# Optimization experiments

Hardware: AMD Instinct MI355X
Metric: run time of the kernel (lower is better)

Reference implementation:

```python
import jax, jax.numpy as jnp
import numpy as np

THRESHOLD = 0.5
NEG_POS_RATIO = 3
ALPHA = 1.0
B, P, C, O = 128, 8732, 21, 32


def xy_to_cxcy(xy):
    return jnp.concatenate([(xy[..., 2:] + xy[..., :2]) / 2, xy[..., 2:] - xy[..., :2]], axis=-1)


def cxcy_to_xy(cxcy):
    return jnp.concatenate([cxcy[..., :2] - cxcy[..., 2:] / 2, cxcy[..., :2] + cxcy[..., 2:] / 2], axis=-1)


def cxcy_to_gcxgcy(cxcy, priors_cxcy):
    g_cxcy = (cxcy[..., :2] - priors_cxcy[..., :2]) / (priors_cxcy[..., 2:] / 10.0)
    g_wh = jnp.log(cxcy[..., 2:] / priors_cxcy[..., 2:]) * 5.0
    return jnp.concatenate([g_cxcy, g_wh], axis=-1)


def find_jaccard_overlap(set1, set2):
    # set1: [O,4] xy, set2: [P,4] xy -> [O,P]
    lo = jnp.maximum(set1[:, None, :2], set2[None, :, :2])
    hi = jnp.minimum(set1[:, None, 2:], set2[None, :, 2:])
    inter = jnp.prod(jnp.clip(hi - lo, 0.0), axis=-1)
    a1 = jnp.prod(set1[:, 2:] - set1[:, :2], axis=-1)
    a2 = jnp.prod(set2[:, 2:] - set2[:, :2], axis=-1)
    union = a1[:, None] + a2[None, :] - inter
    return inter / union


def setup_inputs() -> dict:
    key = jax.random.key(0)
    k0, k1, k2, k3, k4, k5, k6 = jax.random.split(key, 7)
    predicted_locs = jax.random.normal(k0, (B, P, 4), jnp.float32)
    predicted_scores = jax.random.normal(k1, (B, P, C), jnp.float32)
    centers = jax.random.uniform(k2, (B, O, 2), jnp.float32, 0.2, 0.8)
    sizes = jax.random.uniform(k3, (B, O, 2), jnp.float32, 0.05, 0.3)
    boxes = jnp.concatenate([centers - sizes / 2, centers + sizes / 2], axis=-1)
    labels = jax.random.randint(k4, (B, O), 0, C)
    p_c = jax.random.uniform(k5, (P, 2), jnp.float32, 0.05, 0.95)
    p_wh = jax.random.uniform(k6, (P, 2), jnp.float32, 0.05, 0.5)
    priors_cxcy = jnp.concatenate([p_c, p_wh], axis=-1)
    return {"predicted_locs": predicted_locs, "predicted_scores": predicted_scores,
            "boxes": boxes, "labels": labels, "priors_cxcy": priors_cxcy}


def reference(predicted_locs, predicted_scores, boxes, labels, priors_cxcy):
    priors_xy = cxcy_to_xy(priors_cxcy)

    def match_one(boxes_i, labels_i):
        overlap = find_jaccard_overlap(boxes_i, priors_xy)           # [O,P]
        overlap_for_each_prior = jnp.max(overlap, axis=0)            # [P]
        object_for_each_prior = jnp.argmax(overlap, axis=0)          # [P]
        prior_for_each_object = jnp.argmax(overlap, axis=1)          # [O]
        object_for_each_prior = object_for_each_prior.at[prior_for_each_object].set(jnp.arange(O))
        overlap_for_each_prior = overlap_for_each_prior.at[prior_for_each_object].set(1.0)
        label_for_each_prior = labels_i[object_for_each_prior]
        label_for_each_prior = jnp.where(overlap_for_each_prior < THRESHOLD, 0, label_for_each_prior)
        true_locs_i = cxcy_to_gcxgcy(xy_to_cxcy(boxes_i[object_for_each_prior]), priors_cxcy)
        return label_for_each_prior, true_locs_i

    true_classes, true_locs = jax.vmap(match_one)(boxes, labels)     # [B,P], [B,P,4]

    positive = true_classes != 0                                     # [B,P]
    n_positives = jnp.sum(positive, axis=1)                          # [B]
    n_pos_total = jnp.sum(n_positives)

    # L1Loss (mean over selected positive elements, 4 per prior)
    abs_diff = jnp.abs(predicted_locs - true_locs)                   # [B,P,4]
    loc_loss = jnp.sum(abs_diff * positive[..., None]) / (n_pos_total.astype(jnp.float32) * 4.0)

    # per-element cross-entropy
    log_p = jax.nn.log_softmax(predicted_scores, axis=-1)            # [B,P,C]
    conf_loss_all = -jnp.take_along_axis(log_p, true_classes[..., None], axis=-1)[..., 0]  # [B,P]

    conf_loss_pos_sum = jnp.sum(jnp.where(positive, conf_loss_all, 0.0))
    conf_loss_neg = jnp.where(positive, 0.0, conf_loss_all)
    conf_loss_neg_sorted = -jnp.sort(-conf_loss_neg, axis=1)         # descending
    n_hard = NEG_POS_RATIO * n_positives                             # [B]
    hard_mask = jnp.arange(P)[None, :] < n_hard[:, None]             # [B,P]
    conf_loss_hard_neg_sum = jnp.sum(jnp.where(hard_mask, conf_loss_neg_sorted, 0.0))

    conf_loss = (conf_loss_hard_neg_sum + conf_loss_pos_sum) / n_pos_total.astype(jnp.float32)
    return conf_loss + ALPHA * loc_loss
```

## Files before the change

kernel.cpp:

```cpp
#include <hip/hip_runtime.h>
#include <hip/hip_bf16.h>

#define NB 128
#define NP 8732
#define NO 32
#define NC 21
#define PCHUNK 2183


__global__ __launch_bounds__(256) void k_init(int* ws) {
    int i = blockIdx.x * 256 + threadIdx.x;
    const int n = 36352 / 4;
    if (i < n) ws[i] = 0;
}

__global__ __launch_bounds__(256) void k_match_prior(const float* __restrict__ boxes,
                                                     const float* __restrict__ priors,
                                                     int* __restrict__ code) {
    int b = blockIdx.y;
    int base = blockIdx.x * 1024 + threadIdx.x;

    __shared__ float4 sbox[NO];
    if (threadIdx.x < NO)
        sbox[threadIdx.x] = ((const float4*)(boxes + (size_t)b * NO * 4))[threadIdx.x];
    __syncthreads();

    int   pidx[4];
    float px1[4], py1[4], px2[4], py2[4], pa[4];
    float bestv[4];
    int   besto[4];
#pragma unroll
    for (int j = 0; j < 4; ++j) {
        int p = base + 256 * j;
        pidx[j] = p;
        int pp = p < NP ? p : NP - 1;
        float4 pr = ((const float4*)priors)[pp];
        px1[j] = pr.x - pr.z * 0.5f; py1[j] = pr.y - pr.w * 0.5f;
        px2[j] = pr.x + pr.z * 0.5f; py2[j] = pr.y + pr.w * 0.5f;
        pa[j]  = (px2[j] - px1[j]) * (py2[j] - py1[j]);
        bestv[j] = -1.0f; besto[j] = 0;
    }

    for (int o = 0; o < NO; ++o) {
        float4 bx = sbox[o];
        float a1 = (bx.z - bx.x) * (bx.w - bx.y);
#pragma unroll
        for (int j = 0; j < 4; ++j) {
            float lx = fmaxf(bx.x, px1[j]), ly = fmaxf(bx.y, py1[j]);
            float hx = fminf(bx.z, px2[j]), hy = fminf(bx.w, py2[j]);
            float iw = fmaxf(hx - lx, 0.0f), ih = fmaxf(hy - ly, 0.0f);
            float inter = iw * ih;
            float iou = inter / (a1 + pa[j] - inter);
            if (iou > bestv[j]) { bestv[j] = iou; besto[j] = o; }
        }
    }
#pragma unroll
    for (int j = 0; j < 4; ++j)
        if (pidx[j] < NP)
            code[(size_t)b * NP + pidx[j]] = besto[j] | (bestv[j] >= 0.5f ? 256 : 0);
}

__global__ __launch_bounds__(256) void k_match_obj(const float* __restrict__ boxes,
                                                   const float* __restrict__ priors,
                                                   unsigned long long* __restrict__ packed) {
    __shared__ float4 spri[PCHUNK];
    int b = blockIdx.y;
    int pbeg = blockIdx.x * PCHUNK;
    int n = NP - pbeg; if (n > PCHUNK) n = PCHUNK;

    for (int i = threadIdx.x; i < n; i += 256) {
        float4 pr = ((const float4*)priors)[pbeg + i];
        float x1 = pr.x - pr.z * 0.5f, y1 = pr.y - pr.w * 0.5f;
        float x2 = pr.x + pr.z * 0.5f, y2 = pr.y + pr.w * 0.5f;
        spri[i] = make_float4(x1, y1, x2, y2);
    }
    __syncthreads();

    int wid = threadIdx.x >> 6, lane = threadIdx.x & 63;
#pragma unroll
    for (int oo = 0; oo < 8; ++oo) {
        int o = wid * 8 + oo;
        float4 bx = ((const float4*)boxes)[b * NO + o];
        float a1 = (bx.z - bx.x) * (bx.w - bx.y);
        unsigned long long pk = 0ull;
        for (int i = lane; i < n; i += 64) {
            float4 pr = spri[i];
            float lx = fmaxf(bx.x, pr.x), ly = fmaxf(bx.y, pr.y);
            float hx = fminf(bx.z, pr.z), hy = fminf(bx.w, pr.w);
            float iw = fmaxf(hx - lx, 0.0f), ih = fmaxf(hy - ly, 0.0f);
            float inter = iw * ih;
            float pa = (pr.z - pr.x) * (pr.w - pr.y);
            float iou = inter / (a1 + pa - inter);
            unsigned long long key =
                ((unsigned long long)__float_as_uint(iou) << 32) |
                (unsigned long long)(0xFFFFFFFFu - (unsigned)(pbeg + i));
            if (key > pk) pk = key;
        }
        for (int s = 32; s > 0; s >>= 1) {
            unsigned long long t = __shfl_xor(pk, s, 64);
            if (t > pk) pk = t;
        }
        if (lane == 0) atomicMax(&packed[b * NO + o], pk);
    }
}

__global__ void k_force(int* __restrict__ code,
                        const unsigned long long* __restrict__ packed) {
    int b = threadIdx.x;
    if (b >= NB) return;
    unsigned long long pk[NO];
#pragma unroll
    for (int o = 0; o < NO; ++o) pk[o] = packed[b * NO + o];
#pragma unroll
    for (int o = 0; o < NO; ++o) {
        unsigned p = 0xFFFFFFFFu - (unsigned)(pk[o] & 0xFFFFFFFFull);
        if (p < NP) code[(size_t)b * NP + p] = o | 256;
    }
}

__global__ __launch_bounds__(256) void k_loss(const float* __restrict__ plocs,
                                              const float* __restrict__ scores,
                                              const float* __restrict__ boxes,
                                              const int* __restrict__ labels,
                                              const float* __restrict__ priors,
                                              const int* __restrict__ code,
                                              float* __restrict__ confneg,
                                              int* __restrict__ npos,
                                              double* __restrict__ accb) {
    __shared__ float srow[256 * NC];
    int b = blockIdx.y;
    int p0 = blockIdx.x * 256;
    int cnt = NP - p0; if (cnt > 256) cnt = 256;
    int nf4 = cnt * NC / 4;
    const float4* src4 = (const float4*)(scores + ((size_t)b * NP + p0) * NC);
    for (int i = threadIdx.x; i < nf4; i += 256)
        ((float4*)srow)[i] = src4[i];
    __syncthreads();

    int p = p0 + threadIdx.x;
    float posconf = 0.0f, locpart = 0.0f;
    int isp = 0;

    if (p < NP) {
        int cd = code[(size_t)b * NP + p];
        int obj = cd & 255;
        int lbl = (cd & 256) ? labels[b * NO + obj] : 0;

        const float* s = srow + threadIdx.x * NC;
        float m = s[0];
#pragma unroll
        for (int c = 1; c < NC; ++c) m = fmaxf(m, s[c]);
        float sum = 0.0f;
#pragma unroll
        for (int c = 0; c < NC; ++c) sum += __expf(s[c] - m);
        float conf = m + __logf(sum) - s[lbl];

        if (lbl != 0) {
            isp = 1;
            posconf = conf;
            float4 bx = ((const float4*)boxes)[b * NO + obj];
            float4 pr = ((const float4*)priors)[p];
            float cx = (bx.x + bx.z) * 0.5f, cy = (bx.y + bx.w) * 0.5f;
            float w = bx.z - bx.x, h = bx.w - bx.y;
            float gx = (cx - pr.x) / (pr.z * 0.1f);
            float gy = (cy - pr.y) / (pr.w * 0.1f);
            float gw = __logf(w / pr.z) * 5.0f;
            float gh = __logf(h / pr.w) * 5.0f;
            float4 pl = ((const float4*)plocs)[(size_t)b * NP + p];
            locpart = fabsf(pl.x - gx) + fabsf(pl.y - gy) +
                      fabsf(pl.z - gw) + fabsf(pl.w - gh);
        }
        confneg[(size_t)b * NP + p] = isp ? 0.0f : conf;
    }

    for (int s = 32; s > 0; s >>= 1) {
        posconf += __shfl_xor(posconf, s, 64);
        locpart += __shfl_xor(locpart, s, 64);
        isp     += __shfl_xor(isp, s, 64);
    }
    __shared__ float w0[4], w1[4];
    __shared__ int wc[4];
    int wid = threadIdx.x >> 6, lane = threadIdx.x & 63;
    if (lane == 0) { w0[wid] = posconf; w1[wid] = locpart; wc[wid] = isp; }
    __syncthreads();
    if (threadIdx.x == 0) {
        float t0 = w0[0] + w0[1] + w0[2] + w0[3];
        float t1 = w1[0] + w1[1] + w1[2] + w1[3];
        int   tc = wc[0] + wc[1] + wc[2] + wc[3];
        atomicAdd(&npos[b], tc);
        atomicAdd(&accb[b * 3 + 0], (double)t0);
        atomicAdd(&accb[b * 3 + 1], (double)t1);
    }
}

__global__ __launch_bounds__(1024) void k_topk(const float* __restrict__ confneg,
                                               const int* __restrict__ npos,
                                               double* __restrict__ accb) {
    __shared__ int   si[16];
    __shared__ double sd[16];
    __shared__ int   sbcast;
    int tid = threadIdx.x, b = blockIdx.x;
    int lane = tid & 63, wid = tid >> 6;

    const float* src = confneg + (size_t)b * NP;
    float val[9];
#pragma unroll
    for (int j = 0; j < 9; ++j) {
        int i = tid + j * 1024;
        val[j] = (i < NP) ? src[i] : 0.0f;
    }
    int k = npos[b] * 3;
    if (k > NP) k = NP;
    if (k <= 0) return;

    unsigned T = 0;
    for (int bit = 30; bit >= 0; --bit) {
        unsigned cand = T | (1u << bit);
        int cnt = 0;
#pragma unroll
        for (int j = 0; j < 9; ++j)
            cnt += (__float_as_uint(val[j]) >= cand) ? 1 : 0;
        for (int s = 32; s > 0; s >>= 1) cnt += __shfl_xor(cnt, s, 64);
        if (lane == 0) si[wid] = cnt;
        __syncthreads();
        if (tid == 0) {
            int t = 0;
            for (int w = 0; w < 16; ++w) t += si[w];
            sbcast = t;
        }
        __syncthreads();
        if (sbcast >= k) T = cand;
    }

    int cgt = 0;
    double sgt = 0.0;
#pragma unroll
    for (int j = 0; j < 9; ++j) {
        unsigned u = __float_as_uint(val[j]);
        if (u > T) { cgt++; sgt += (double)val[j]; }
    }
    for (int s = 32; s > 0; s >>= 1) {
        cgt += __shfl_xor(cgt, s, 64);
        sgt += __shfl_xor(sgt, s, 64);
    }
    if (lane == 0) { si[wid] = cgt; sd[wid] = sgt; }
    __syncthreads();
    if (tid == 0) {
        int cg = 0; double sg = 0.0;
        for (int w = 0; w < 16; ++w) { cg += si[w]; sg += sd[w]; }
        accb[b * 3 + 2] = sg + (double)(k - cg) * (double)__uint_as_float(T);
    }
}

__global__ __launch_bounds__(128) void k_final(const int* __restrict__ npos,
                                               const double* __restrict__ accb,
                                               float* __restrict__ out) {
    int b = threadIdx.x;
    double pc = accb[b * 3 + 0];
    double lc = accb[b * 3 + 1];
    double hn = accb[b * 3 + 2];
    double np_ = (double)npos[b];
    for (int s = 32; s > 0; s >>= 1) {
        pc  += __shfl_xor(pc, s, 64);
        lc  += __shfl_xor(lc, s, 64);
        hn  += __shfl_xor(hn, s, 64);
        np_ += __shfl_xor(np_, s, 64);
    }
    __shared__ double sD[4][2];
    int wid = threadIdx.x >> 6, lane = threadIdx.x & 63;
    if (lane == 0) { sD[0][wid] = pc; sD[1][wid] = lc; sD[2][wid] = hn; sD[3][wid] = np_; }
    __syncthreads();
    if (threadIdx.x == 0) {
        double P = sD[0][0] + sD[0][1];
        double L = sD[1][0] + sD[1][1];
        double H = sD[2][0] + sD[2][1];
        double nt = sD[3][0] + sD[3][1];
        out[0] = (float)((H + P) / nt + L / (nt * 4.0));
    }
}

extern "C" void kernel_launch(void* const* d_in, const int* in_sizes, int n_in,
                              void* d_out, int out_size, void* d_ws, size_t ws_size,
                              hipStream_t stream) {
    const float* plocs  = (const float*)d_in[0];
    const float* scores = (const float*)d_in[1];
    const float* boxes  = (const float*)d_in[2];
    const int*   labels = (const int*)d_in[3];
    const float* priors = (const float*)d_in[4];
    float* out = (float*)d_out;

    char* ws = (char*)d_ws;
    unsigned long long* packed = (unsigned long long*)ws;
    int*    npos    = (int*)(ws + 32768);
    double* accb    = (double*)(ws + 33280);
    int*    code    = (int*)(ws + 36352);
    float*  confneg = (float*)(ws + 36352 + (size_t)NB * NP * 4);

    hipLaunchKernelGGL(k_init, dim3((36352 / 4 + 255) / 256), dim3(256), 0, stream, (int*)ws);
    hipLaunchKernelGGL(k_match_prior, dim3((NP + 1023) / 1024, NB), dim3(256), 0, stream,
                       boxes, priors, code);
    hipLaunchKernelGGL(k_match_obj, dim3(4, NB), dim3(256), 0, stream,
                       boxes, priors, packed);
    hipLaunchKernelGGL(k_force, dim3(1), dim3(128), 0, stream, code, packed);
    hipLaunchKernelGGL(k_loss, dim3((NP + 255) / 256, NB), dim3(256), 0, stream,
                       plocs, scores, boxes, labels, priors, code, confneg, npos, accb);
    hipLaunchKernelGGL(k_topk, dim3(NB), dim3(1024), 0, stream, confneg, npos, accb);
    hipLaunchKernelGGL(k_final, dim3(1), dim3(128), 0, stream, npos, accb, out);
}
```

Measured before the change: 269.0 us.

## Fuse prior matching into loss kernel and collapse pipeline into three launches

Per-prior best-object matching moves into the loss kernel, and the forced-match overrides are applied from the packed per-object argmax values held in shared memory. This removes the code array round-trip through global memory and the k_match_prior and k_force launches. Per-object matching now runs as one block per batch that loops over all prior chunks and writes results directly, without atomics. That same kernel zeroes the workspace, so k_init is gone. The final reduction is merged into the top-k kernel through a last-block atomic counter, in exchange for fewer blocks in the object-matching pass and a serialized tail in the last block.

```diff
diff --git a/kernel.cpp b/kernel.cpp
--- a/kernel.cpp
+++ b/kernel.cpp
@@ -5,116 +5,66 @@
 #define NP 8732
 #define NO 32
 #define NC 21
-#define PCHUNK 2183
-
-
-__global__ __launch_bounds__(256) void k_init(int* ws) {
-    int i = blockIdx.x * 256 + threadIdx.x;
-    const int n = 36352 / 4;
-    if (i < n) ws[i] = 0;
-}
-
-__global__ __launch_bounds__(256) void k_match_prior(const float* __restrict__ boxes,
-                                                     const float* __restrict__ priors,
-                                                     int* __restrict__ code) {
-    int b = blockIdx.y;
-    int base = blockIdx.x * 1024 + threadIdx.x;
-
+#define CPB 2183
+
+
+__global__ __launch_bounds__(512) void k_obj(const float* __restrict__ boxes,
+                                             const float* __restrict__ priors,
+                                             unsigned long long* __restrict__ packed,
+                                             int* __restrict__ npos,
+                                             double* __restrict__ accb,
+                                             int* __restrict__ flag) {
+    __shared__ float4 spri[CPB];
     __shared__ float4 sbox[NO];
-    if (threadIdx.x < NO)
-        sbox[threadIdx.x] = ((const float4*)(boxes + (size_t)b * NO * 4))[threadIdx.x];
-    __syncthreads();
-
-    int   pidx[4];
-    float px1[4], py1[4], px2[4], py2[4], pa[4];
-    float bestv[4];
-    int   besto[4];
-#pragma unroll
-    for (int j = 0; j < 4; ++j) {
-        int p = base + 256 * j;
-        pidx[j] = p;
-        int pp = p < NP ? p : NP - 1;
-        float4 pr = ((const float4*)priors)[pp];
-        px1[j] = pr.x - pr.z * 0.5f; py1[j] = pr.y - pr.w * 0.5f;
-        px2[j] = pr.x + pr.z * 0.5f; py2[j] = pr.y + pr.w * 0.5f;
-        pa[j]  = (px2[j] - px1[j]) * (py2[j] - py1[j]);
-        bestv[j] = -1.0f; besto[j] = 0;
-    }
-
-    for (int o = 0; o < NO; ++o) {
-        float4 bx = sbox[o];
-        float a1 = (bx.z - bx.x) * (bx.w - bx.y);
-#pragma unroll
-        for (int j = 0; j < 4; ++j) {
-            float lx = fmaxf(bx.x, px1[j]), ly = fmaxf(bx.y, py1[j]);
-            float hx = fminf(bx.z, px2[j]), hy = fminf(bx.w, py2[j]);
-            float iw = fmaxf(hx - lx, 0.0f), ih = fmaxf(hy - ly, 0.0f);
-            float inter = iw * ih;
-            float iou = inter / (a1 + pa[j] - inter);
-            if (iou > bestv[j]) { bestv[j] = iou; besto[j] = o; }
-        }
-    }
-#pragma unroll
-    for (int j = 0; j < 4; ++j)
-        if (pidx[j] < NP)
-            code[(size_t)b * NP + pidx[j]] = besto[j] | (bestv[j] >= 0.5f ? 256 : 0);
-}
-
-__global__ __launch_bounds__(256) void k_match_obj(const float* __restrict__ boxes,
-                                                   const float* __restrict__ priors,
-                                                   unsigned long long* __restrict__ packed) {
-    __shared__ float4 spri[PCHUNK];
-    int b = blockIdx.y;
-    int pbeg = blockIdx.x * PCHUNK;
-    int n = NP - pbeg; if (n > PCHUNK) n = PCHUNK;
-
-    for (int i = threadIdx.x; i < n; i += 256) {
-        float4 pr = ((const float4*)priors)[pbeg + i];
-        float x1 = pr.x - pr.z * 0.5f, y1 = pr.y - pr.w * 0.5f;
-        float x2 = pr.x + pr.z * 0.5f, y2 = pr.y + pr.w * 0.5f;
-        spri[i] = make_float4(x1, y1, x2, y2);
-    }
-    __syncthreads();
-
-    int wid = threadIdx.x >> 6, lane = threadIdx.x & 63;
-#pragma unroll
-    for (int oo = 0; oo < 8; ++oo) {
-        int o = wid * 8 + oo;
-        float4 bx = ((const float4*)boxes)[b * NO + o];
-        float a1 = (bx.z - bx.x) * (bx.w - bx.y);
-        unsigned long long pk = 0ull;
-        for (int i = lane; i < n; i += 64) {
-            float4 pr = spri[i];
-            float lx = fmaxf(bx.x, pr.x), ly = fmaxf(bx.y, pr.y);
-            float hx = fminf(bx.z, pr.z), hy = fminf(bx.w, pr.w);
-            float iw = fmaxf(hx - lx, 0.0f), ih = fmaxf(hy - ly, 0.0f);
-            float inter = iw * ih;
-            float pa = (pr.z - pr.x) * (pr.w - pr.y);
-            float iou = inter / (a1 + pa - inter);
-            unsigned long long key =
-                ((unsigned long long)__float_as_uint(iou) << 32) |
-                (unsigned long long)(0xFFFFFFFFu - (unsigned)(pbeg + i));
-            if (key > pk) pk = key;
-        }
+    const int b = blockIdx.x, tid = threadIdx.x;
+    const int lane = tid & 63, wid = tid >> 6;
+
+    if (tid == 0) npos[b] = 0;
+    if (tid >= 1 && tid <= 3) accb[b * 3 + (tid - 1)] = 0.0;
+    if (b == 0 && tid == 4) *flag = 0;
+    if (tid < NO) sbox[tid] = ((const float4*)boxes)[b * NO + tid];
+
+    unsigned long long key[4] = {0ull, 0ull, 0ull, 0ull};
+
+    for (int ch = 0; ch < 4; ++ch) {
+        const int pbeg = ch * CPB;
+        __syncthreads();
+        for (int i = tid; i < CPB; i += 512) {
+            float4 pr = ((const float4*)priors)[pbeg + i];
+            spri[i] = make_float4(pr.x - pr.z * 0.5f, pr.y - pr.w * 0.5f,
+                                  pr.x + pr.z * 0.5f, pr.y + pr.w * 0.5f);
+        }
+        __syncthreads();
+#pragma unroll
+        for (int oo = 0; oo < 4; ++oo) {
+            const int o = wid * 4 + oo;
+            float4 bx = sbox[o];
+            float a1 = (bx.z - bx.x) * (bx.w - bx.y);
+            unsigned long long pk = key[oo];
+            for (int i = lane; i < CPB; i += 64) {
+                float4 pr = spri[i];
+                float lx = fmaxf(bx.x, pr.x), ly = fmaxf(bx.y, pr.y);
+                float hx = fminf(bx.z, pr.z), hy = fminf(bx.w, pr.w);
+                float iw = fmaxf(hx - lx, 0.0f), ih = fmaxf(hy - ly, 0.0f);
+                float inter = iw * ih;
+                float pa = (pr.z - pr.x) * (pr.w - pr.y);
+                float iou = inter / (a1 + pa - inter);
+                unsigned long long k2 =
+                    ((unsigned long long)__float_as_uint(iou) << 32) |
+                    (unsigned long long)(0xFFFFFFFFu - (unsigned)(pbeg + i));
+                if (k2 > pk) pk = k2;
+            }
+            key[oo] = pk;
+        }
+    }
+#pragma unroll
+    for (int oo = 0; oo < 4; ++oo) {
+        unsigned long long pk = key[oo];
         for (int s = 32; s > 0; s >>= 1) {
             unsigned long long t = __shfl_xor(pk, s, 64);
             if (t > pk) pk = t;
         }
-        if (lane == 0) atomicMax(&packed[b * NO + o], pk);
-    }
-}
-
-__global__ void k_force(int* __restrict__ code,
-                        const unsigned long long* __restrict__ packed) {
-    int b = threadIdx.x;
-    if (b >= NB) return;
-    unsigned long long pk[NO];
-#pragma unroll
-    for (int o = 0; o < NO; ++o) pk[o] = packed[b * NO + o];
-#pragma unroll
-    for (int o = 0; o < NO; ++o) {
-        unsigned p = 0xFFFFFFFFu - (unsigned)(pk[o] & 0xFFFFFFFFull);
-        if (p < NP) code[(size_t)b * NP + p] = o | 256;
+        if (lane == 0) packed[b * NO + wid * 4 + oo] = pk;
     }
 }
 
@@ -123,30 +73,63 @@
                                               const float* __restrict__ boxes,
                                               const int* __restrict__ labels,
                                               const float* __restrict__ priors,
-                                              const int* __restrict__ code,
+                                              const unsigned long long* __restrict__ packed,
                                               float* __restrict__ confneg,
                                               int* __restrict__ npos,
                                               double* __restrict__ accb) {
     __shared__ float srow[256 * NC];
-    int b = blockIdx.y;
-    int p0 = blockIdx.x * 256;
-    int cnt = NP - p0; if (cnt > 256) cnt = 256;
-    int nf4 = cnt * NC / 4;
+    __shared__ float4 sbox[NO];
+    __shared__ int sfp[NO];
+    __shared__ int slab[NO];
+    const int b = blockIdx.y, tid = threadIdx.x;
+    const int p0 = blockIdx.x * 256;
+    const int cnt = min(256, NP - p0);
+
+    if (tid < NO) {
+        sbox[tid] = ((const float4*)boxes)[b * NO + tid];
+        slab[tid] = labels[b * NO + tid];
+        unsigned long long pk = packed[b * NO + tid];
+        sfp[tid] = (int)(0xFFFFFFFFu - (unsigned)(pk & 0xFFFFFFFFull));
+    }
+    const int nf4 = cnt * NC / 4;
     const float4* src4 = (const float4*)(scores + ((size_t)b * NP + p0) * NC);
-    for (int i = threadIdx.x; i < nf4; i += 256)
-        ((float4*)srow)[i] = src4[i];
+    for (int i = tid; i < nf4; i += 256) ((float4*)srow)[i] = src4[i];
     __syncthreads();
 
-    int p = p0 + threadIdx.x;
     float posconf = 0.0f, locpart = 0.0f;
     int isp = 0;
 
-    if (p < NP) {
-        int cd = code[(size_t)b * NP + p];
-        int obj = cd & 255;
-        int lbl = (cd & 256) ? labels[b * NO + obj] : 0;
-
-        const float* s = srow + threadIdx.x * NC;
+    if (tid < cnt) {
+        const int p = p0 + tid;
+        float4 pr = ((const float4*)priors)[p];
+        float px1 = pr.x - pr.z * 0.5f, py1 = pr.y - pr.w * 0.5f;
+        float px2 = pr.x + pr.z * 0.5f, py2 = pr.y + pr.w * 0.5f;
+        float pa = (px2 - px1) * (py2 - py1);
+
+        float bestv = -1.0f;
+        int besto = 0;
+#pragma unroll
+        for (int o = 0; o < NO; ++o) {
+            float4 bx = sbox[o];
+            float a1 = (bx.z - bx.x) * (bx.w - bx.y);
+            float lx = fmaxf(bx.x, px1), ly = fmaxf(bx.y, py1);
+            float hx = fminf(bx.z, px2), hy = fminf(bx.w, py2);
+            float iw = fmaxf(hx - lx, 0.0f), ih = fmaxf(hy - ly, 0.0f);
+            float inter = iw * ih;
+            float iou = inter / (a1 + pa - inter);
+            if (iou > bestv) { bestv = iou; besto = o; }
+        }
+        int ovr = -1;
+#pragma unroll
+        for (int o = 0; o < NO; ++o)
+            if (sfp[o] == p) ovr = o;
+
+        int obj, matched;
+        if (ovr >= 0) { obj = ovr; matched = 1; }
+        else          { obj = besto; matched = (bestv >= 0.5f) ? 1 : 0; }
+        int lbl = matched ? slab[obj] : 0;
+
+        const float* s = srow + tid * NC;
         float m = s[0];
 #pragma unroll
         for (int c = 1; c < NC; ++c) m = fmaxf(m, s[c]);
@@ -158,8 +141,7 @@
         if (lbl != 0) {
             isp = 1;
             posconf = conf;
-            float4 bx = ((const float4*)boxes)[b * NO + obj];
-            float4 pr = ((const float4*)priors)[p];
+            float4 bx = sbox[obj];
             float cx = (bx.x + bx.z) * 0.5f, cy = (bx.y + bx.w) * 0.5f;
             float w = bx.z - bx.x, h = bx.w - bx.y;
             float gx = (cx - pr.x) / (pr.z * 0.1f);
@@ -180,27 +162,26 @@
     }
     __shared__ float w0[4], w1[4];
     __shared__ int wc[4];
-    int wid = threadIdx.x >> 6, lane = threadIdx.x & 63;
+    int wid = tid >> 6, lane = tid & 63;
     if (lane == 0) { w0[wid] = posconf; w1[wid] = locpart; wc[wid] = isp; }
     __syncthreads();
-    if (threadIdx.x == 0) {
-        float t0 = w0[0] + w0[1] + w0[2] + w0[3];
-        float t1 = w1[0] + w1[1] + w1[2] + w1[3];
-        int   tc = wc[0] + wc[1] + wc[2] + wc[3];
-        atomicAdd(&npos[b], tc);
-        atomicAdd(&accb[b * 3 + 0], (double)t0);
-        atomicAdd(&accb[b * 3 + 1], (double)t1);
-    }
-}
-
-__global__ __launch_bounds__(1024) void k_topk(const float* __restrict__ confneg,
-                                               const int* __restrict__ npos,
-                                               double* __restrict__ accb) {
+    if (tid == 0) {
+        atomicAdd(&npos[b], wc[0] + wc[1] + wc[2] + wc[3]);
+        atomicAdd(&accb[b * 3 + 0], (double)(w0[0] + w0[1] + w0[2] + w0[3]));
+        atomicAdd(&accb[b * 3 + 1], (double)(w1[0] + w1[1] + w1[2] + w1[3]));
+    }
+}
+
+__global__ __launch_bounds__(1024) void k_topk_final(const float* __restrict__ confneg,
+                                                     const int* __restrict__ npos,
+                                                     double* __restrict__ accb,
+                                                     int* __restrict__ flag,
+                                                     float* __restrict__ out) {
     __shared__ int   si[16];
     __shared__ double sd[16];
-    __shared__ int   sbcast;
-    int tid = threadIdx.x, b = blockIdx.x;
-    int lane = tid & 63, wid = tid >> 6;
+    __shared__ int   sbcast, slast;
+    const int tid = threadIdx.x, b = blockIdx.x;
+    const int lane = tid & 63, wid = tid >> 6;
 
     const float* src = confneg + (size_t)b * NP;
     float val[9];
@@ -211,71 +192,76 @@
     }
     int k = npos[b] * 3;
     if (k > NP) k = NP;
-    if (k <= 0) return;
-
-    unsigned T = 0;
-    for (int bit = 30; bit >= 0; --bit) {
-        unsigned cand = T | (1u << bit);
-        int cnt = 0;
-#pragma unroll
-        for (int j = 0; j < 9; ++j)
-            cnt += (__float_as_uint(val[j]) >= cand) ? 1 : 0;
-        for (int s = 32; s > 0; s >>= 1) cnt += __shfl_xor(cnt, s, 64);
-        if (lane == 0) si[wid] = cnt;
+
+    if (k > 0) {
+        unsigned T = 0;
+        for (int bit = 30; bit >= 0; --bit) {
+            unsigned cand = T | (1u << bit);
+            int cnt = 0;
+#pragma unroll
+            for (int j = 0; j < 9; ++j)
+                cnt += (__float_as_uint(val[j]) >= cand) ? 1 : 0;
+            for (int s = 32; s > 0; s >>= 1) cnt += __shfl_xor(cnt, s, 64);
+            if (lane == 0) si[wid] = cnt;
+            __syncthreads();
+            if (tid == 0) {
+                int t = 0;
+                for (int w = 0; w < 16; ++w) t += si[w];
+                sbcast = t;
+            }
+            __syncthreads();
+            if (sbcast >= k) T = cand;
+        }
+        int cgt = 0;
+        double sgt = 0.0;
+#pragma unroll
+        for (int j = 0; j < 9; ++j) {
+            unsigned u = __float_as_uint(val[j]);
+            if (u > T) { cgt++; sgt += (double)val[j]; }
+        }
+        for (int s = 32; s > 0; s >>= 1) {
+            cgt += __shfl_xor(cgt, s, 64);
+            sgt += __shfl_xor(sgt, s, 64);
+        }
+        if (lane == 0) { si[wid] = cgt; sd[wid] = sgt; }
         __syncthreads();
         if (tid == 0) {
-            int t = 0;
-            for (int w = 0; w < 16; ++w) t += si[w];
-            sbcast = t;
-        }
-        __syncthreads();
-        if (sbcast >= k) T = cand;
-    }
-
-    int cgt = 0;
-    double sgt = 0.0;
-#pragma unroll
-    for (int j = 0; j < 9; ++j) {
-        unsigned u = __float_as_uint(val[j]);
-        if (u > T) { cgt++; sgt += (double)val[j]; }
-    }
-    for (int s = 32; s > 0; s >>= 1) {
-        cgt += __shfl_xor(cgt, s, 64);
-        sgt += __shfl_xor(sgt, s, 64);
-    }
-    if (lane == 0) { si[wid] = cgt; sd[wid] = sgt; }
+            int cg = 0; double sg = 0.0;
+            for (int w = 0; w < 16; ++w) { cg += si[w]; sg += sd[w]; }
+            accb[b * 3 + 2] = sg + (double)(k - cg) * (double)__uint_as_float(T);
+        }
+    }
+
+    __threadfence();
+    if (tid == 0) slast = (atomicAdd(flag, 1) == NB - 1) ? 1 : 0;
     __syncthreads();
-    if (tid == 0) {
-        int cg = 0; double sg = 0.0;
-        for (int w = 0; w < 16; ++w) { cg += si[w]; sg += sd[w]; }
-        accb[b * 3 + 2] = sg + (double)(k - cg) * (double)__uint_as_float(T);
-    }
-}
-
-__global__ __launch_bounds__(128) void k_final(const int* __restrict__ npos,
-                                               const double* __restrict__ accb,
-                                               float* __restrict__ out) {
-    int b = threadIdx.x;
-    double pc = accb[b * 3 + 0];
-    double lc = accb[b * 3 + 1];
-    double hn = accb[b * 3 + 2];
-    double np_ = (double)npos[b];
-    for (int s = 32; s > 0; s >>= 1) {
-        pc  += __shfl_xor(pc, s, 64);
-        lc  += __shfl_xor(lc, s, 64);
-        hn  += __shfl_xor(hn, s, 64);
-        np_ += __shfl_xor(np_, s, 64);
-    }
-    __shared__ double sD[4][2];
-    int wid = threadIdx.x >> 6, lane = threadIdx.x & 63;
-    if (lane == 0) { sD[0][wid] = pc; sD[1][wid] = lc; sD[2][wid] = hn; sD[3][wid] = np_; }
-    __syncthreads();
-    if (threadIdx.x == 0) {
-        double P = sD[0][0] + sD[0][1];
-        double L = sD[1][0] + sD[1][1];
-        double H = sD[2][0] + sD[2][1];
-        double nt = sD[3][0] + sD[3][1];
-        out[0] = (float)((H + P) / nt + L / (nt * 4.0));
+    if (slast) {
+        __threadfence();
+        double pc = 0, lc = 0, hn = 0, nn = 0;
+        if (tid < NB) {
+            pc = accb[tid * 3 + 0];
+            lc = accb[tid * 3 + 1];
+            hn = accb[tid * 3 + 2];
+            nn = (double)npos[tid];
+        }
+        if (tid < 128) {
+            for (int s = 32; s > 0; s >>= 1) {
+                pc += __shfl_xor(pc, s, 64);
+                lc += __shfl_xor(lc, s, 64);
+                hn += __shfl_xor(hn, s, 64);
+                nn += __shfl_xor(nn, s, 64);
+            }
+            if (lane == 0) { sd[wid * 4 + 0] = pc; sd[wid * 4 + 1] = lc;
+                             sd[wid * 4 + 2] = hn; sd[wid * 4 + 3] = nn; }
+        }
+        __syncthreads();
+        if (tid == 0) {
+            double P  = sd[0] + sd[4];
+            double L  = sd[1] + sd[5];
+            double H  = sd[2] + sd[6];
+            double NT = sd[3] + sd[7];
+            out[0] = (float)((H + P) / NT + L / (NT * 4.0));
+        }
     }
 }
 
@@ -293,17 +279,13 @@
     unsigned long long* packed = (unsigned long long*)ws;
     int*    npos    = (int*)(ws + 32768);
     double* accb    = (double*)(ws + 33280);
-    int*    code    = (int*)(ws + 36352);
-    float*  confneg = (float*)(ws + 36352 + (size_t)NB * NP * 4);
-
-    hipLaunchKernelGGL(k_init, dim3((36352 / 4 + 255) / 256), dim3(256), 0, stream, (int*)ws);
-    hipLaunchKernelGGL(k_match_prior, dim3((NP + 1023) / 1024, NB), dim3(256), 0, stream,
-                       boxes, priors, code);
-    hipLaunchKernelGGL(k_match_obj, dim3(4, NB), dim3(256), 0, stream,
-                       boxes, priors, packed);
-    hipLaunchKernelGGL(k_force, dim3(1), dim3(128), 0, stream, code, packed);
+    int*    flag    = (int*)(ws + 36352);
+    float*  confneg = (float*)(ws + 36608);
+
+    hipLaunchKernelGGL(k_obj, dim3(NB), dim3(512), 0, stream,
+                       boxes, priors, packed, npos, accb, flag);
     hipLaunchKernelGGL(k_loss, dim3((NP + 255) / 256, NB), dim3(256), 0, stream,
-                       plocs, scores, boxes, labels, priors, code, confneg, npos, accb);
-    hipLaunchKernelGGL(k_topk, dim3(NB), dim3(1024), 0, stream, confneg, npos, accb);
-    hipLaunchKernelGGL(k_final, dim3(1), dim3(128), 0, stream, npos, accb, out);
-}
+                       plocs, scores, boxes, labels, priors, packed, confneg, npos, accb);
+    hipLaunchKernelGGL(k_topk_final, dim3(NB), dim3(1024), 0, stream,
+                       confneg, npos, accb, flag, out);
+}
```

New measurement: 312.3 us. +16.1%, slower.
